# Kernel tuning notes

Hardware: AMD Instinct MI355X
Metric: run time of the kernel (lower is better)

## Reference

```python
import jax, jax.numpy as jnp
import numpy as np

B, F, L, P = 64, 512, 512, 96
HT, HF = 8, 8  # temporal / feature attention heads
EPS_ATTN = 1e-6
EPS_LN = 1e-5
EPS_REVIN = 1e-5


def _layernorm(x, g, b):
    m = x.mean(axis=-1, keepdims=True)
    v = x.var(axis=-1, keepdims=True)
    return (x - m) / jnp.sqrt(v + EPS_LN) * g + b


def _lin_attn(x, Wq, bq, Wk, bk, Wv, bv, Wo, bo, H):
    # x: (B, N, D). Katharopoulos linear attention with elu+1 feature map.
    Bz, N, D = x.shape
    hd = D // H

    def proj(W, b):
        return (x @ W.T + b).reshape(Bz, N, H, hd).transpose(0, 2, 1, 3)  # (B,H,N,hd)

    Q = jax.nn.elu(proj(Wq, bq)) + 1.0
    K = jax.nn.elu(proj(Wk, bk)) + 1.0
    V = proj(Wv, bv)
    KV = jnp.einsum('bhnd,bhne->bhde', K, V)           # (B,H,hd,hd)
    out = jnp.einsum('bhnd,bhde->bhne', Q, KV)         # (B,H,N,hd)
    Z = K.sum(axis=2)                                  # (B,H,hd)
    norm = jnp.einsum('bhnd,bhd->bhn', Q, Z)[..., None] + EPS_ATTN
    out = (out / norm).transpose(0, 2, 1, 3).reshape(Bz, N, D)
    return out @ Wo.T + bo


def setup_inputs() -> dict:
    key = jax.random.key(0)
    ks = jax.random.split(key, 32)
    s = 0.1  # xavier-ish gain

    def w(k, shape, fan):
        return jax.random.normal(k, shape, dtype=jnp.float32) * (s / np.sqrt(fan))

    inp = {
        'x': jax.random.normal(ks[0], (B, F, L), dtype=jnp.float32),
        # RevIN affine
        'rg': jnp.ones((1, 1, F), jnp.float32),
        'rb': jnp.zeros((1, 1, F), jnp.float32),
        # LayerNorms
        'n1g': jnp.ones((F,), jnp.float32), 'n1b': jnp.zeros((F,), jnp.float32),
        'n2g': jnp.ones((L,), jnp.float32), 'n2b': jnp.zeros((L,), jnp.float32),
        # temporal attention (dim=F)
        'tWq': w(ks[1], (F, F), F), 'tbq': jnp.zeros((F,), jnp.float32),
        'tWk': w(ks[2], (F, F), F), 'tbk': jnp.zeros((F,), jnp.float32),
        'tWv': w(ks[3], (F, F), F), 'tbv': jnp.zeros((F,), jnp.float32),
        'tWo': w(ks[4], (F, F), F), 'tbo': jnp.zeros((F,), jnp.float32),
        # feature attention (dim=L)
        'fWq': w(ks[5], (L, L), L), 'fbq': jnp.zeros((L,), jnp.float32),
        'fWk': w(ks[6], (L, L), L), 'fbk': jnp.zeros((L,), jnp.float32),
        'fWv': w(ks[7], (L, L), L), 'fbv': jnp.zeros((L,), jnp.float32),
        'fWo': w(ks[8], (L, L), L), 'fbo': jnp.zeros((L,), jnp.float32),
        # individual per-feature Linear bank: seq_len -> pred_len
        'Wlin': w(ks[9], (F, P, L), L), 'blin': jnp.zeros((F, P), jnp.float32),
        # projector F -> 1
        'Wproj': w(ks[10], (1, F), F), 'bproj': jnp.zeros((1,), jnp.float32),
    }
    return inp


def reference(x, rg, rb, n1g, n1b,
              tWq, tbq, tWk, tbk, tWv, tbv, tWo, tbo,
              n2g, n2b,
              fWq, fbq, fWk, fbk, fWv, fbv, fWo, fbo,
              Wlin, blin, Wproj, bproj):
    # (B, F, L) -> (B, L, F)
    h = x.transpose(0, 2, 1)
    # RevIN norm (stats detached, std is unbiased like torch.std)
    mean = jax.lax.stop_gradient(h.mean(axis=1, keepdims=True))
    std = jax.lax.stop_gradient(jnp.std(h, axis=1, keepdims=True, ddof=1) + EPS_REVIN)
    h = (h - mean) / std * rg + rb

    # Dual linear attention
    r = h
    h = _layernorm(h, n1g, n1b)
    h = _lin_attn(h, tWq, tbq, tWk, tbk, tWv, tbv, tWo, tbo, HT) + r
    h = h.transpose(0, 2, 1)  # (B, F, L)
    r = h
    h = _layernorm(h, n2g, n2b)
    h = _lin_attn(h, fWq, fbq, fWk, fbk, fWv, fbv, fWo, fbo, HF) + r
    # (module transposes back to (B,L,F) then LinearCrypto permutes to (B,F,L);
    #  we stay in (B,F,L))

    # individual per-feature linear: seq_len -> pred_len
    y = jnp.einsum('bfl,fpl->bfp', h, Wlin) + blin[None]  # (B,F,P)
    y = y.transpose(0, 2, 1)                              # (B,P,F)
    # RevIN denorm
    y = (y - rb) / rg
    y = y * std + mean
    # projector F -> 1
    out = y @ Wproj.T + bproj  # (B,P,1)
    return out[..., 0]
```

## Files before the change

### kernel.cpp

```cpp
#include <hip/hip_runtime.h>
#include <hip/hip_bf16.h>
#include <cstdint>
#include <cstddef>


#define EPS_ATTN 1e-6f
#define EPS_LN   1e-5f
#define EPS_REVIN 1e-5f

typedef __attribute__((ext_vector_type(8))) short bf16x8;
typedef __attribute__((ext_vector_type(4))) float f32x4;
typedef __attribute__((ext_vector_type(8))) unsigned short u16x8;

__device__ __forceinline__ float bf2f(unsigned short u) {
  unsigned int x = ((unsigned int)u) << 16;
  return __builtin_bit_cast(float, x);
}
__device__ __forceinline__ unsigned short f2bf(float f) {
  __hip_bfloat16 h = __float2bfloat16(f);
  return __builtin_bit_cast(unsigned short, h);
}
__device__ __forceinline__ void gload16(const void* g, void* l) {
  __builtin_amdgcn_global_load_lds(
      (const __attribute__((address_space(1))) void*)g,
      (__attribute__((address_space(3))) void*)l, 16, 0, 0);
}

__global__ __launch_bounds__(256) void revin_xn_k(const float* __restrict__ x,
                                                  const float* __restrict__ rg,
                                                  const float* __restrict__ rb,
                                                  float* __restrict__ meanb,
                                                  float* __restrict__ stdb,
                                                  unsigned short* __restrict__ xn) {
  int wid = threadIdx.x >> 6, lane = threadIdx.x & 63;
  int row = blockIdx.x * 4 + wid;
  const float* xr = x + (size_t)row * 512 + lane * 8;
  float4 a = *(const float4*)xr;
  float4 c = *(const float4*)(xr + 4);
  float s1 = a.x + a.y + a.z + a.w + c.x + c.y + c.z + c.w;
  float s2 = a.x * a.x + a.y * a.y + a.z * a.z + a.w * a.w +
             c.x * c.x + c.y * c.y + c.z * c.z + c.w * c.w;
#pragma unroll
  for (int off = 1; off < 64; off <<= 1) { s1 += __shfl_xor(s1, off); s2 += __shfl_xor(s2, off); }
  float m = s1 * (1.f / 512.f);
  float var = fmaxf((s2 - 512.f * m * m) * (1.f / 511.f), 0.f);
  float sd = sqrtf(var) + EPS_REVIN;
  int f = row & 511;
  float sc = rg[f] / sd;
  float of = rb[f] - m * sc;
  u16x8 o;
  o[0] = f2bf(a.x * sc + of); o[1] = f2bf(a.y * sc + of);
  o[2] = f2bf(a.z * sc + of); o[3] = f2bf(a.w * sc + of);
  o[4] = f2bf(c.x * sc + of); o[5] = f2bf(c.y * sc + of);
  o[6] = f2bf(c.z * sc + of); o[7] = f2bf(c.w * sc + of);
  *(u16x8*)(xn + (size_t)row * 512 + lane * 8) = o;
  if (lane == 0) { meanb[row] = m; stdb[row] = sd; }
}

__global__ __launch_bounds__(256) void tln_k(const unsigned short* __restrict__ xn,
                                             const float* __restrict__ g,
                                             const float* __restrict__ bq,
                                             unsigned short* __restrict__ o16) {
  __shared__ unsigned short Ts[32][528] __attribute__((aligned(16)));
  const int b = blockIdx.y, l0 = blockIdx.x * 32;
  const int tid = threadIdx.x;
#pragma unroll
  for (int it = 0; it < 8; ++it) {
    int idx = it * 256 + tid;
    int f = idx >> 2, lc = (idx & 3) * 8;
    u16x8 v = *(const u16x8*)(xn + ((size_t)b * 512 + f) * 512 + l0 + lc);
#pragma unroll
    for (int j = 0; j < 8; ++j) Ts[lc + j][f] = v[j];
  }
  __syncthreads();
  const int l = tid >> 3, q = tid & 7;
  float s1 = 0.f, s2 = 0.f;
#pragma unroll
  for (int i = 0; i < 8; ++i) {
    int c = (i + q) & 7;
    bf16x8 t = *(const bf16x8*)&Ts[l][q * 64 + c * 8];
#pragma unroll
    for (int j = 0; j < 8; ++j) {
      float x = bf2f((unsigned short)t[j]);
      s1 += x; s2 += x * x;
    }
  }
#pragma unroll
  for (int off = 1; off < 8; off <<= 1) { s1 += __shfl_xor(s1, off); s2 += __shfl_xor(s2, off); }
  float m = s1 * (1.f / 512.f);
  float var = fmaxf(s2 * (1.f / 512.f) - m * m, 0.f);
  float iv = 1.f / sqrtf(var + EPS_LN);
#pragma unroll
  for (int i = 0; i < 8; ++i) {
    int c = (i + q) & 7;
    int f8 = q * 64 + c * 8;
    bf16x8 t = *(const bf16x8*)&Ts[l][f8];
    float4 g0 = *(const float4*)(g + f8);
    float4 g1 = *(const float4*)(g + f8 + 4);
    float4 b0 = *(const float4*)(bq + f8);
    float4 b1 = *(const float4*)(bq + f8 + 4);
    u16x8 o;
    o[0] = f2bf((bf2f((unsigned short)t[0]) - m) * iv * g0.x + b0.x);
    o[1] = f2bf((bf2f((unsigned short)t[1]) - m) * iv * g0.y + b0.y);
    o[2] = f2bf((bf2f((unsigned short)t[2]) - m) * iv * g0.z + b0.z);
    o[3] = f2bf((bf2f((unsigned short)t[3]) - m) * iv * g0.w + b0.w);
    o[4] = f2bf((bf2f((unsigned short)t[4]) - m) * iv * g1.x + b1.x);
    o[5] = f2bf((bf2f((unsigned short)t[5]) - m) * iv * g1.y + b1.y);
    o[6] = f2bf((bf2f((unsigned short)t[6]) - m) * iv * g1.z + b1.z);
    o[7] = f2bf((bf2f((unsigned short)t[7]) - m) * iv * g1.w + b1.w);
    *(u16x8*)&Ts[l][f8] = o;
  }
  __syncthreads();
#pragma unroll
  for (int it = 0; it < 8; ++it) {
    int idx = it * 256 + tid;
    int ll = idx >> 6, f8 = (idx & 63) * 8;
    u16x8 v = *(const u16x8*)&Ts[ll][f8];
    *(u16x8*)(o16 + ((size_t)b * 512 + l0 + ll) * 512 + f8) = v;
  }
}

__global__ __launch_bounds__(256) void ln_k(const unsigned short* __restrict__ in,
                                            const float* __restrict__ g,
                                            const float* __restrict__ bq,
                                            unsigned short* __restrict__ o16) {
  int row = blockIdx.x * 4 + (threadIdx.x >> 6);
  int lane = threadIdx.x & 63;
  u16x8 u = *(const u16x8*)(in + (size_t)row * 512 + lane * 8);
  float v[8];
#pragma unroll
  for (int j = 0; j < 8; ++j) v[j] = bf2f(u[j]);
  float s1 = 0.f, s2 = 0.f;
#pragma unroll
  for (int j = 0; j < 8; ++j) { s1 += v[j]; s2 += v[j] * v[j]; }
#pragma unroll
  for (int off = 1; off < 64; off <<= 1) { s1 += __shfl_xor(s1, off); s2 += __shfl_xor(s2, off); }
  float m = s1 * (1.f / 512.f);
  float var = fmaxf(s2 * (1.f / 512.f) - m * m, 0.f);
  float iv = 1.f / sqrtf(var + EPS_LN);
  float4 g0 = *(const float4*)(g + lane * 8);
  float4 g1 = *(const float4*)(g + lane * 8 + 4);
  float4 b0 = *(const float4*)(bq + lane * 8);
  float4 b1 = *(const float4*)(bq + lane * 8 + 4);
  u16x8 o;
  o[0] = f2bf((v[0] - m) * iv * g0.x + b0.x);
  o[1] = f2bf((v[1] - m) * iv * g0.y + b0.y);
  o[2] = f2bf((v[2] - m) * iv * g0.z + b0.z);
  o[3] = f2bf((v[3] - m) * iv * g0.w + b0.w);
  o[4] = f2bf((v[4] - m) * iv * g1.x + b1.x);
  o[5] = f2bf((v[5] - m) * iv * g1.y + b1.y);
  o[6] = f2bf((v[6] - m) * iv * g1.z + b1.z);
  o[7] = f2bf((v[7] - m) * iv * g1.w + b1.w);
  *(u16x8*)(o16 + (size_t)row * 512 + lane * 8) = o;
}

__global__ __launch_bounds__(256) void wconv_k(const float* w0, const float* w1,
                                               const float* w2, const float* w3,
                                               const float* w4, const float* w5,
                                               const float* w6, const float* w7,
                                               unsigned short* __restrict__ out) {
  const float* srcs[8] = {w0, w1, w2, w3, w4, w5, w6, w7};
  const float* s = srcs[blockIdx.y];
  size_t idx = (size_t)blockIdx.x * 2048 + threadIdx.x * 8;
  float4 v0 = *(const float4*)(s + idx);
  float4 v1 = *(const float4*)(s + idx + 4);
  u16x8 o;
  o[0] = f2bf(v0.x); o[1] = f2bf(v0.y); o[2] = f2bf(v0.z); o[3] = f2bf(v0.w);
  o[4] = f2bf(v1.x); o[5] = f2bf(v1.y); o[6] = f2bf(v1.z); o[7] = f2bf(v1.w);
  *(u16x8*)(out + (size_t)blockIdx.y * 262144 + idx) = o;
}

__device__ __forceinline__ void stage32(const unsigned short* __restrict__ src,
                                        unsigned short* dst, int tid, int koff) {
#pragma unroll
  for (int c = 0; c < 2; ++c) {
    int idx = c * 256 + tid;
    int line = idx >> 3, s8 = idx & 7;
    int logical = s8 ^ (line & 7);
    int srow = line * 2 + (logical >> 2);
    int gs = logical & 3;
    gload16(src + (size_t)srow * 512 + koff + gs * 8, dst + idx * 8);
  }
}

__device__ __forceinline__ void gemm_core(const unsigned short* __restrict__ A,
                                          const unsigned short* __restrict__ W,
                                          unsigned short* smem,
                                          f32x4 (&acc)[4][4],
                                          int m0, int wrow, int tid) {
  const int w = tid >> 6, lane = tid & 63;
  const int wr = w >> 1, wc = w & 1;
  const int r16 = lane & 15, g = lane >> 4;
  const unsigned short* Ag = A + (size_t)m0 * 512;
  const unsigned short* Wg = W + (size_t)wrow * 512;

  stage32(Ag, smem, tid, 0);
  stage32(Wg, smem + 4096, tid, 0);
  for (int t = 0; t < 16; ++t) {
    unsigned short* bufA = smem + (t & 1) * 8192;
    unsigned short* bufB = bufA + 4096;
    asm volatile("s_barrier" ::: "memory");
    if (t < 15) {
      unsigned short* nA = smem + ((t & 1) ^ 1) * 8192;
      stage32(Ag, nA, tid, (t + 1) * 32);
      stage32(Wg, nA + 4096, tid, (t + 1) * 32);
      asm volatile("s_waitcnt vmcnt(4)" ::: "memory");
    } else {
      asm volatile("s_waitcnt vmcnt(0)" ::: "memory");
    }
    asm volatile("s_barrier" ::: "memory");
    bf16x8 fa[4], fb[4];
#pragma unroll
    for (int i = 0; i < 4; ++i) {
      int row = wr * 64 + i * 16 + r16;
      int line = row >> 1;
      int phys = ((((row & 1) << 2) | g) ^ (line & 7));
      fa[i] = *(const bf16x8*)&bufA[line * 64 + phys * 8];
      int rowb = wc * 64 + i * 16 + r16;
      int lineb = rowb >> 1;
      int physb = ((((rowb & 1) << 2) | g) ^ (lineb & 7));
      fb[i] = *(const bf16x8*)&bufB[lineb * 64 + physb * 8];
    }
#pragma unroll
    for (int i = 0; i < 4; ++i)
#pragma unroll
      for (int j = 0; j < 4; ++j)
        acc[i][j] = __builtin_amdgcn_mfma_f32_16x16x32_bf16(fa[i], fb[j], acc[i][j], 0, 0, 0);
  }
  __syncthreads();
}

template <int TRANS, int ACT, int RES>
__device__ __forceinline__ void gemm_epilogue(f32x4 (&acc)[4][4],
                                              unsigned short* Cs,
                                              const float* __restrict__ bias,
                                              const unsigned short* __restrict__ resid,
                                              unsigned short* __restrict__ out,
                                              int m0, int n0, int tid) {
  const int w = tid >> 6, lane = tid & 63;
  const int wr = w >> 1, wc = w & 1;
  const int ro = (lane >> 4) * 4, c16 = lane & 15;
#pragma unroll
  for (int j = 0; j < 4; ++j) {
    int nl = wc * 64 + j * 16 + c16;
    float bi = bias[n0 + nl];
#pragma unroll
    for (int i = 0; i < 4; ++i) {
      int ml = wr * 64 + i * 16 + ro;
#pragma unroll
      for (int r = 0; r < 4; ++r) {
        float v = acc[i][j][r] + bi;
        if constexpr (ACT) v = (v > 0.f) ? v + 1.f : __expf(v);
        if constexpr (TRANS) Cs[nl * 136 + ml + r] = f2bf(v);
        else                 Cs[(ml + r) * 136 + nl] = f2bf(v);
      }
    }
  }
  __syncthreads();
  size_t rowbase; int colbase;
  if constexpr (TRANS) { rowbase = (size_t)((m0 >> 9) * 512 + n0); colbase = m0 & 511; }
  else                 { rowbase = (size_t)m0; colbase = n0; }
#pragma unroll
  for (int c = 0; c < 8; ++c) {
    int idx = c * 256 + tid;
    int rr = idx >> 4, c8 = (idx & 15) * 8;
    u16x8 v = *(const u16x8*)&Cs[rr * 136 + c8];
    size_t gaddr = (rowbase + rr) * 512 + colbase + c8;
    if constexpr (RES) {
      u16x8 rv = *(const u16x8*)(resid + gaddr);
#pragma unroll
      for (int q = 0; q < 8; ++q) v[q] = f2bf(bf2f(v[q]) + bf2f(rv[q]));
    }
    *(u16x8*)(out + gaddr) = v;
  }
}

template <int TRANS, int ACT, int RES>
__global__ __launch_bounds__(256, 4) void gemm_std_k(const unsigned short* __restrict__ A,
                                                     const unsigned short* __restrict__ W,
                                                     const float* __restrict__ bias,
                                                     const unsigned short* __restrict__ resid,
                                                     unsigned short* __restrict__ out) {
  __shared__ unsigned short smem[17408] __attribute__((aligned(16)));
  const int tid = threadIdx.x;
  const int bid = blockIdx.x;
  const int nb = (bid & 7) * 128 + (bid >> 3);
  const int m0 = (nb >> 2) * 128;
  const int n0 = (nb & 3) * 128;
  f32x4 acc[4][4] = {};
  gemm_core(A, W, smem, acc, m0, n0, tid);
  gemm_epilogue<TRANS, ACT, RES>(acc, smem, bias, resid, out, m0, n0, tid);
}

__global__ __launch_bounds__(256, 4) void gemm_qkv3_k(const unsigned short* __restrict__ A,
                                                      const unsigned short* __restrict__ Wqkv,
                                                      const float* __restrict__ bq,
                                                      const float* __restrict__ bk,
                                                      const float* __restrict__ bv,
                                                      unsigned short* __restrict__ Q,
                                                      unsigned short* __restrict__ K,
                                                      unsigned short* __restrict__ V) {
  __shared__ unsigned short smem[17408] __attribute__((aligned(16)));
  const int tid = threadIdx.x;
  const unsigned int bid = blockIdx.x;
  const unsigned int nb = (bid & 7) * 384 + (bid >> 3);
  const int mi = nb / 12, ni = nb % 12;
  const int m0 = mi * 128;
  const int mat = ni >> 2;
  const int n0 = (ni & 3) * 128;
  f32x4 acc[4][4] = {};
  gemm_core(A, Wqkv, smem, acc, m0, mat * 512 + n0, tid);

  const float* bias = (mat == 0) ? bq : (mat == 1) ? bk : bv;
  unsigned short* out = (mat == 0) ? Q : (mat == 1) ? K : V;
  const bool trans = (mat > 0);
  const bool act = (mat < 2);

  const int w = tid >> 6, lane = tid & 63;
  const int wr = w >> 1, wc = w & 1;
  const int ro = (lane >> 4) * 4, c16 = lane & 15;
  unsigned short* Cs = smem;
#pragma unroll
  for (int j = 0; j < 4; ++j) {
    int nl = wc * 64 + j * 16 + c16;
    float bi = bias[n0 + nl];
#pragma unroll
    for (int i = 0; i < 4; ++i) {
      int ml = wr * 64 + i * 16 + ro;
#pragma unroll
      for (int r = 0; r < 4; ++r) {
        float v = acc[i][j][r] + bi;
        if (act) v = (v > 0.f) ? v + 1.f : __expf(v);
        int row = trans ? nl : (ml + r);
        int col = trans ? (ml + r) : nl;
        Cs[row * 136 + col] = f2bf(v);
      }
    }
  }
  __syncthreads();
  size_t rowbase = trans ? (size_t)((m0 >> 9) * 512 + n0) : (size_t)m0;
  int colbase = trans ? (m0 & 511) : n0;
#pragma unroll
  for (int c = 0; c < 8; ++c) {
    int idx = c * 256 + tid;
    int rr = idx >> 4, c8 = (idx & 15) * 8;
    u16x8 v = *(const u16x8*)&Cs[rr * 136 + c8];
    *(u16x8*)(out + (rowbase + rr) * 512 + colbase + c8) = v;
  }
}

__global__ __launch_bounds__(256) void kv_attn_k(unsigned short* __restrict__ Q16,
                                                 const unsigned short* __restrict__ KT,
                                                 const unsigned short* __restrict__ VT) {
  __shared__ unsigned short kvs[4096] __attribute__((aligned(16)));
  __shared__ float Zs[64];
  const int bh = blockIdx.x, b = bh >> 3, h = bh & 7;
  const int tid = threadIdx.x, w = tid >> 6, lane = tid & 63;
  const int r16 = lane & 15, g = lane >> 4;

  const unsigned short* vb = VT + ((size_t)bh * 64 + w * 16 + r16) * 512 + g * 8;
  const unsigned short* kb = KT + ((size_t)bh * 64 + r16) * 512 + g * 8;
  const short ob = (short)0x3F80;
  const bf16x8 onesf = {ob, ob, ob, ob, ob, ob, ob, ob};
  f32x4 acc[4] = {}, zacc[4] = {};
  for (int n0 = 0; n0 < 512; n0 += 32) {
    bf16x8 vf = *(const bf16x8*)(vb + n0);
#pragma unroll
    for (int j = 0; j < 4; ++j) {
      bf16x8 kf = *(const bf16x8*)(kb + (size_t)j * 16 * 512 + n0);
      acc[j] = __builtin_amdgcn_mfma_f32_16x16x32_bf16(vf, kf, acc[j], 0, 0, 0);
      zacc[j] = __builtin_amdgcn_mfma_f32_16x16x32_bf16(onesf, kf, zacc[j], 0, 0, 0);
    }
  }
#pragma unroll
  for (int j = 0; j < 4; ++j)
#pragma unroll
    for (int r = 0; r < 4; ++r) {
      int e = w * 16 + g * 4 + r, d = j * 16 + r16;
      int byte = e * 128 + ((((d >> 3) ^ (e & 7)) << 4)) + (d & 7) * 2;
      *(unsigned short*)((char*)kvs + byte) = f2bf(acc[j][r]);
    }
  if (w == 0 && g == 0) {
#pragma unroll
    for (int j = 0; j < 4; ++j) Zs[j * 16 + r16] = zacc[j][0];
  }
  __syncthreads();

#pragma unroll
  for (int i = 0; i < 8; ++i) {
    int mrow = b * 512 + w * 128 + i * 16;
    const unsigned short* qrow = Q16 + (size_t)(mrow + r16) * 512 + h * 64;
    bf16x8 q0 = *(const bf16x8*)(qrow + g * 8);
    bf16x8 q1 = *(const bf16x8*)(qrow + 32 + g * 8);
    float np = 0.f;
#pragma unroll
    for (int q = 0; q < 8; ++q) np = fmaf(bf2f((unsigned short)q0[q]), Zs[g * 8 + q], np);
#pragma unroll
    for (int q = 0; q < 8; ++q) np = fmaf(bf2f((unsigned short)q1[q]), Zs[32 + g * 8 + q], np);
    f32x4 a2[4] = {};
#pragma unroll
    for (int j = 0; j < 4; ++j) {
      int e = j * 16 + r16;
      int byte0 = e * 128, sw = (e & 7) << 4;
      bf16x8 k0 = *(const bf16x8*)((char*)kvs + ((byte0 + g * 16) ^ sw));
      bf16x8 k1 = *(const bf16x8*)((char*)kvs + ((byte0 + 64 + g * 16) ^ sw));
      a2[j] = __builtin_amdgcn_mfma_f32_16x16x32_bf16(q0, k0, a2[j], 0, 0, 0);
      a2[j] = __builtin_amdgcn_mfma_f32_16x16x32_bf16(q1, k1, a2[j], 0, 0, 0);
    }
    np += __shfl_xor(np, 16);
    np += __shfl_xor(np, 32);
    float inv = 1.f / (np + EPS_ATTN);
    float inv4[4];
#pragma unroll
    for (int r = 0; r < 4; ++r) inv4[r] = __shfl(inv, g * 4 + r);
    int orow0 = mrow + g * 4;
#pragma unroll
    for (int j = 0; j < 4; ++j)
#pragma unroll
      for (int r = 0; r < 4; ++r)
        Q16[(size_t)(orow0 + r) * 512 + h * 64 + j * 16 + r16] = f2bf(a2[j][r] * inv4[r]);
  }
}

__global__ __launch_bounds__(256) void feat_linear_k(const unsigned short* __restrict__ h3,
                                                     const float* __restrict__ Wlin,
                                                     const float* __restrict__ blin,
                                                     float* __restrict__ Y) {
  __shared__ unsigned short As[64 * 64] __attribute__((aligned(16)));
  __shared__ unsigned short Bs[96 * 64] __attribute__((aligned(16)));
  const int f = blockIdx.x;
  const int tid = threadIdx.x;
  const int w = tid >> 6, lane = tid & 63;
  const int r16 = lane & 15, g = lane >> 4;
  const int r8 = lane >> 3, s8 = lane & 7, gs = s8 ^ r8;

  f32x4 acc[6] = {};
  for (int k0 = 0; k0 < 512; k0 += 64) {
#pragma unroll
    for (int c = 0; c < 2; ++c) {
      int row = w * 16 + c * 8 + r8;
      gload16(h3 + ((size_t)row * 512 + f) * 512 + k0 + gs * 8,
              As + (w * 16 + c * 8) * 64);
    }
#pragma unroll
    for (int it = 0; it < 3; ++it) {
      int idx = it * 256 + tid;
      int pp = idx >> 3, sl = idx & 7;
      const float* src = Wlin + ((size_t)f * 96 + pp) * 512 + k0 + sl * 8;
      float4 v0 = *(const float4*)src;
      float4 v1 = *(const float4*)(src + 4);
      u16x8 o;
      o[0] = f2bf(v0.x); o[1] = f2bf(v0.y); o[2] = f2bf(v0.z); o[3] = f2bf(v0.w);
      o[4] = f2bf(v1.x); o[5] = f2bf(v1.y); o[6] = f2bf(v1.z); o[7] = f2bf(v1.w);
      *(u16x8*)&Bs[pp * 64 + (sl ^ (pp & 7)) * 8] = o;
    }
    __syncthreads();
#pragma unroll
    for (int s = 0; s < 2; ++s) {
      int arow = w * 16 + r16;
      bf16x8 fa = *(const bf16x8*)&As[arow * 64 + (((s * 4 + g) ^ (arow & 7)) * 8)];
#pragma unroll
      for (int n = 0; n < 6; ++n) {
        int brow = n * 16 + r16;
        bf16x8 fb = *(const bf16x8*)&Bs[brow * 64 + (((s * 4 + g) ^ (brow & 7)) * 8)];
        acc[n] = __builtin_amdgcn_mfma_f32_16x16x32_bf16(fa, fb, acc[n], 0, 0, 0);
      }
    }
    __syncthreads();
  }
  const int b0 = w * 16 + g * 4;
#pragma unroll
  for (int n = 0; n < 6; ++n) {
    float bi = blin[f * 96 + n * 16 + r16];
#pragma unroll
    for (int r = 0; r < 4; ++r)
      Y[((size_t)(b0 + r) * 512 + f) * 96 + n * 16 + r16] = acc[n][r] + bi;
  }
}

__global__ __launch_bounds__(256) void final_out_k(const float* __restrict__ Y,
                                                   const float* __restrict__ meanb,
                                                   const float* __restrict__ stdb,
                                                   const float* __restrict__ rg,
                                                   const float* __restrict__ rb,
                                                   const float* __restrict__ Wproj,
                                                   const float* __restrict__ bproj,
                                                   float* __restrict__ out) {
  int b = blockIdx.x;
  __shared__ float cs[512];
  __shared__ float kred[4];
  int t = threadIdx.x;
  float kpart = 0.f;
  for (int f = t; f < 512; f += 256) {
    float sd = stdb[b * 512 + f], mn = meanb[b * 512 + f];
    float g = rg[f], rbv = rb[f], wp = Wproj[f];
    float c = wp * sd / g;
    cs[f] = c;
    kpart += wp * mn - c * rbv;
  }
#pragma unroll
  for (int off = 32; off; off >>= 1) kpart += __shfl_down(kpart, off);
  int wid = t >> 6, lane = t & 63;
  if (lane == 0) kred[wid] = kpart;
  __syncthreads();
  float K = kred[0] + kred[1] + kred[2] + kred[3] + bproj[0];
  if (t < 96) {
    float acc = 0.f;
    for (int f = 0; f < 512; ++f) acc = fmaf(cs[f], Y[((size_t)b * 512 + f) * 96 + t], acc);
    out[b * 96 + t] = acc + K;
  }
}

extern "C" void kernel_launch(void* const* d_in, const int* in_sizes, int n_in,
                              void* d_out, int out_size, void* d_ws, size_t ws_size,
                              hipStream_t stream) {
  const float* x    = (const float*)d_in[0];
  const float* rg   = (const float*)d_in[1];
  const float* rb   = (const float*)d_in[2];
  const float* n1g  = (const float*)d_in[3];
  const float* n1b  = (const float*)d_in[4];
  const float* n2g  = (const float*)d_in[5];
  const float* n2b  = (const float*)d_in[6];
  const float* tWq  = (const float*)d_in[7];
  const float* tbq  = (const float*)d_in[8];
  const float* tWk  = (const float*)d_in[9];
  const float* tbk  = (const float*)d_in[10];
  const float* tWv  = (const float*)d_in[11];
  const float* tbv  = (const float*)d_in[12];
  const float* tWo  = (const float*)d_in[13];
  const float* tbo  = (const float*)d_in[14];
  const float* fWq  = (const float*)d_in[15];
  const float* fbq  = (const float*)d_in[16];
  const float* fWk  = (const float*)d_in[17];
  const float* fbk  = (const float*)d_in[18];
  const float* fWv  = (const float*)d_in[19];
  const float* fbv  = (const float*)d_in[20];
  const float* fWo  = (const float*)d_in[21];
  const float* fbo  = (const float*)d_in[22];
  const float* Wlin = (const float*)d_in[23];
  const float* blin = (const float*)d_in[24];
  const float* Wprj = (const float*)d_in[25];
  const float* bprj = (const float*)d_in[26];
  float* out = (float*)d_out;

  const size_t SZ = (size_t)64 * 512 * 512;
  char* p = (char*)d_ws;
  unsigned short* xn  = (unsigned short*)p; p += SZ * 2;
  unsigned short* h2  = (unsigned short*)p; p += SZ * 2;
  unsigned short* h3  = (unsigned short*)p; p += SZ * 2;
  unsigned short* abf = (unsigned short*)p; p += SZ * 2;
  unsigned short* q16 = (unsigned short*)p; p += SZ * 2;
  unsigned short* k16 = (unsigned short*)p; p += SZ * 2;
  unsigned short* v16 = (unsigned short*)p; p += SZ * 2;
  unsigned short* wbf = (unsigned short*)p; p += (size_t)8 * 262144 * 2;
  float* meanb = (float*)p;         p += 32768 * 4;
  float* stdb  = (float*)p;         p += 32768 * 4;
  float* ybuf  = (float*)abf;

  wconv_k<<<dim3(128, 8), 256, 0, stream>>>(tWq, tWk, tWv, tWo, fWq, fWk, fWv, fWo, wbf);
  revin_xn_k<<<8192, 256, 0, stream>>>(x, rg, rb, meanb, stdb, xn);

  tln_k<<<dim3(16, 64), 256, 0, stream>>>(xn, n1g, n1b, abf);
  gemm_qkv3_k<<<3072, 256, 0, stream>>>(abf, wbf, tbq, tbk, tbv, q16, k16, v16);
  kv_attn_k<<<512, 256, 0, stream>>>(q16, k16, v16);
  gemm_std_k<1, 0, 1><<<1024, 256, 0, stream>>>(q16, wbf + 3 * 262144, tbo, xn, h2);

  ln_k<<<8192, 256, 0, stream>>>(h2, n2g, n2b, abf);
  gemm_qkv3_k<<<3072, 256, 0, stream>>>(abf, wbf + 4 * 262144, fbq, fbk, fbv, q16, k16, v16);
  kv_attn_k<<<512, 256, 0, stream>>>(q16, k16, v16);
  gemm_std_k<0, 0, 1><<<1024, 256, 0, stream>>>(q16, wbf + 7 * 262144, fbo, h2, h3);

  feat_linear_k<<<512, 256, 0, stream>>>(h3, Wlin, blin, ybuf);
  final_out_k<<<64, 256, 0, stream>>>(ybuf, meanb, stdb, rg, rb, Wprj, bprj, out);
}
```

Baseline: 384.4 us.

## Replace double-buffered K=32 GEMM pipeline with single-buffered K=64 tiles

The GEMM core drops the double-buffered 32-wide K staging, with its manual vmcnt waits and split barriers. It now loads 64-wide K tiles into a single LDS buffer using a per-wave row layout and an XOR swizzle, then runs two MFMA sub-steps per tile between __syncthreads. This halves the number of loop iterations and barriers and simplifies address math. In exchange, global loads no longer overlap with MFMA compute, so memory latency is exposed on every tile.

```diff
diff --git a/kernel.cpp b/kernel.cpp
--- a/kernel.cpp
+++ b/kernel.cpp
@@ -170,19 +170,6 @@
   *(u16x8*)(out + (size_t)blockIdx.y * 262144 + idx) = o;
 }
 
-__device__ __forceinline__ void stage32(const unsigned short* __restrict__ src,
-                                        unsigned short* dst, int tid, int koff) {
-#pragma unroll
-  for (int c = 0; c < 2; ++c) {
-    int idx = c * 256 + tid;
-    int line = idx >> 3, s8 = idx & 7;
-    int logical = s8 ^ (line & 7);
-    int srow = line * 2 + (logical >> 2);
-    int gs = logical & 3;
-    gload16(src + (size_t)srow * 512 + koff + gs * 8, dst + idx * 8);
-  }
-}
-
 __device__ __forceinline__ void gemm_core(const unsigned short* __restrict__ A,
                                           const unsigned short* __restrict__ W,
                                           unsigned short* smem,
@@ -190,44 +177,38 @@
                                           int m0, int wrow, int tid) {
   const int w = tid >> 6, lane = tid & 63;
   const int wr = w >> 1, wc = w & 1;
-  const int r16 = lane & 15, g = lane >> 4;
-  const unsigned short* Ag = A + (size_t)m0 * 512;
-  const unsigned short* Wg = W + (size_t)wrow * 512;
-
-  stage32(Ag, smem, tid, 0);
-  stage32(Wg, smem + 4096, tid, 0);
-  for (int t = 0; t < 16; ++t) {
-    unsigned short* bufA = smem + (t & 1) * 8192;
-    unsigned short* bufB = bufA + 4096;
-    asm volatile("s_barrier" ::: "memory");
-    if (t < 15) {
-      unsigned short* nA = smem + ((t & 1) ^ 1) * 8192;
-      stage32(Ag, nA, tid, (t + 1) * 32);
-      stage32(Wg, nA + 4096, tid, (t + 1) * 32);
-      asm volatile("s_waitcnt vmcnt(4)" ::: "memory");
-    } else {
-      asm volatile("s_waitcnt vmcnt(0)" ::: "memory");
-    }
-    asm volatile("s_barrier" ::: "memory");
-    bf16x8 fa[4], fb[4];
-#pragma unroll
-    for (int i = 0; i < 4; ++i) {
-      int row = wr * 64 + i * 16 + r16;
-      int line = row >> 1;
-      int phys = ((((row & 1) << 2) | g) ^ (line & 7));
-      fa[i] = *(const bf16x8*)&bufA[line * 64 + phys * 8];
-      int rowb = wc * 64 + i * 16 + r16;
-      int lineb = rowb >> 1;
-      int physb = ((((rowb & 1) << 2) | g) ^ (lineb & 7));
-      fb[i] = *(const bf16x8*)&bufB[lineb * 64 + physb * 8];
-    }
-#pragma unroll
-    for (int i = 0; i < 4; ++i)
-#pragma unroll
-      for (int j = 0; j < 4; ++j)
-        acc[i][j] = __builtin_amdgcn_mfma_f32_16x16x32_bf16(fa[i], fb[j], acc[i][j], 0, 0, 0);
-  }
-  __syncthreads();
+  const int r8 = lane >> 3, s8 = lane & 7, gslot = s8 ^ r8;
+  const unsigned short* Ag = A + (size_t)(m0 + w * 32 + r8) * 512 + gslot * 8;
+  const unsigned short* Wg = W + (size_t)(wrow + w * 32 + r8) * 512 + gslot * 8;
+  unsigned short* Asw = smem + w * 2048;
+  unsigned short* Bsw = smem + 8192 + w * 2048;
+  for (int k0 = 0; k0 < 512; k0 += 64) {
+#pragma unroll
+    for (int c = 0; c < 4; ++c) {
+      gload16(Ag + (size_t)c * 8 * 512 + k0, Asw + c * 512);
+      gload16(Wg + (size_t)c * 8 * 512 + k0, Bsw + c * 512);
+    }
+    __syncthreads();
+#pragma unroll
+    for (int s = 0; s < 2; ++s) {
+      bf16x8 fa[4], fb[4];
+#pragma unroll
+      for (int i = 0; i < 4; ++i) {
+        int ra = wr * 64 + i * 16 + (lane & 15);
+        int sa = (s * 4 + (lane >> 4)) ^ (ra & 7);
+        fa[i] = *(const bf16x8*)&smem[ra * 64 + sa * 8];
+        int rb = wc * 64 + i * 16 + (lane & 15);
+        int sb = (s * 4 + (lane >> 4)) ^ (rb & 7);
+        fb[i] = *(const bf16x8*)&smem[8192 + rb * 64 + sb * 8];
+      }
+#pragma unroll
+      for (int i = 0; i < 4; ++i)
+#pragma unroll
+        for (int j = 0; j < 4; ++j)
+          acc[i][j] = __builtin_amdgcn_mfma_f32_16x16x32_bf16(fa[i], fb[j], acc[i][j], 0, 0, 0);
+    }
+    __syncthreads();
+  }
 }
 
 template <int TRANS, int ACT, int RES>
```

Measured after the change: 372.6 us, median of 2. -3.1%, faster.
